# Optimization experiments

Measured on AMD Instinct MI355X. Metric: run time of the kernel, lower is better.

Reference implementation:

```python
import jax, jax.numpy as jnp
import numpy as np

NUM_EMB = 8192
DIM = 64
DECAY = 0.99
EPS = 1e-05
COMMIT = 0.25


def setup_inputs() -> dict:
    key = jax.random.key(0)
    k1, k2, k3 = jax.random.split(key, 3)
    inputs = jax.random.normal(k1, (8, 4096, DIM), jnp.float32)
    weight = jax.random.normal(k2, (NUM_EMB, DIM), jnp.float32)
    ema_cluster_count = jnp.ones((NUM_EMB,), jnp.float32)
    ema_weight_sum = jax.random.normal(k3, (NUM_EMB, DIM), jnp.float32)
    return {
        'inputs': inputs,
        'weight': weight,
        'ema_cluster_count': ema_cluster_count,
        'ema_weight_sum': ema_weight_sum,
    }


def reference(inputs, weight, ema_cluster_count, ema_weight_sum):
    flat = inputs.reshape(-1, DIM)  # [N, D]
    distances = (
        jnp.sum(flat ** 2, axis=1, keepdims=True)
        + jnp.sum(weight ** 2, axis=1)
        - 2.0 * flat @ weight.T
    )
    idx = jnp.argmin(distances, axis=1)  # [N] int

    # EMA stats (training branch): one-hot column sums == segment counts,
    # encodings.T @ flat == segment sums of inputs by code index.
    counts = jax.ops.segment_sum(
        jnp.ones(flat.shape[0], jnp.float32), idx, num_segments=NUM_EMB)
    new_cc = ema_cluster_count * DECAY + (1.0 - DECAY) * counts
    emb_sum = jax.ops.segment_sum(flat, idx, num_segments=NUM_EMB)
    new_ws = ema_weight_sum * DECAY + (1.0 - DECAY) * emb_sum

    n = jnp.sum(new_cc)
    smoothed = (new_cc + EPS) / (n + NUM_EMB * EPS) * n
    new_weight = new_ws / smoothed[:, None]  # updated codebook [K, D]

    quantized_raw = new_weight[idx].reshape(inputs.shape)
    e_latent_loss = jnp.mean((jax.lax.stop_gradient(quantized_raw) - inputs) ** 2)
    vq_loss = COMMIT * e_latent_loss

    avg_probs = counts / flat.shape[0]
    perplexity = jnp.exp(-jnp.sum(avg_probs * jnp.log(avg_probs + 1e-10)))

    # straight-through estimator
    quantized = inputs + jax.lax.stop_gradient(quantized_raw - inputs)
    return quantized, vq_loss, idx, perplexity, new_weight, new_cc, new_ws
```

## Files before the change

### kernel.cpp

```cpp
#include <hip/hip_runtime.h>
#include <math.h>

typedef _Float16 f16x8 __attribute__((ext_vector_type(8)));
typedef float f32x4 __attribute__((ext_vector_type(4)));

#define NROWS 32768
#define KEMB  8192

#define DECAYF 0.99f
#define OMDF   0.01f

#define OUT_Q    0
#define OUT_LOSS 2097152
#define OUT_IDX  2097153
#define OUT_PERP 2129921
#define OUT_NW   2129922
#define OUT_NCC  2654210
#define OUT_NWS  2662402

#define WS_N      0
#define WS_ENT    1
#define WS_COUNTS 4
#define WS_EMB    8196
#define WS_IDX    532484
#define WS_W2H    565252
#define WS_WFRAG  573444
#define WS_ZERO_UNITS 532484

__device__ __forceinline__ float sq_rn(float v) { return __fmul_rn(v, v); }

__device__ __forceinline__ float npsumsq64(const float* vbuf) {
  float a[8];
#pragma unroll
  for (int j = 0; j < 8; ++j) a[j] = sq_rn(vbuf[j]);
#pragma unroll
  for (int m = 1; m < 8; ++m)
#pragma unroll
    for (int j = 0; j < 8; ++j) a[j] = __fadd_rn(a[j], sq_rn(vbuf[m*8 + j]));
  return __fadd_rn(__fadd_rn(__fadd_rn(a[0],a[1]), __fadd_rn(a[2],a[3])),
                   __fadd_rn(__fadd_rn(a[4],a[5]), __fadd_rn(a[6],a[7])));
}

__device__ __forceinline__ void split_f16(float x, _Float16& hi, _Float16& lo) {
  hi = (_Float16)x;
  float r = __fsub_rn(x, (float)hi);
  lo = (_Float16)r;
}

__global__ __launch_bounds__(256) void prep_kernel(const float* __restrict__ wg,
                                                   float* __restrict__ ws) {
  const int tid = blockIdx.x * 256 + threadIdx.x;
  if (tid < KEMB) {
    const float* src = wg + (size_t)tid * 64;
    float vbuf[64];
#pragma unroll
    for (int f = 0; f < 16; ++f) {
      float4 v = *(const float4*)(src + f*4);
      vbuf[f*4+0]=v.x; vbuf[f*4+1]=v.y; vbuf[f*4+2]=v.z; vbuf[f*4+3]=v.w;
    }
    ws[WS_W2H + tid] = __fmul_rn(0.5f, npsumsq64(vbuf));
  } else if (tid < KEMB + 65536) {
    const int u = tid - KEMB;
    const int K = u >> 3, g = u & 7;
    const int n = K & 15, P = K >> 4;
    const int slot = (g&3)*16 + n, shi = g >> 2;
    const float* src = wg + (size_t)K*64 + g*8;
    float4 v0 = *(const float4*)src, v1 = *(const float4*)(src + 4);
    float vv[8] = {v0.x,v0.y,v0.z,v0.w,v1.x,v1.y,v1.z,v1.w};
    f16x8 hi, lo;
#pragma unroll
    for (int j = 0; j < 8; ++j) { _Float16 h, l; split_f16(vv[j], h, l); hi[j]=h; lo[j]=l; }
    _Float16* wf = (_Float16*)(ws + WS_WFRAG);
    *(f16x8*)&wf[((size_t)(P*4 + shi)*64 + slot)*8]     = hi;
    *(f16x8*)&wf[((size_t)(P*4 + 2 + shi)*64 + slot)*8] = lo;
  }
}

__global__ __launch_bounds__(512) void argmin_kernel(const float* __restrict__ xg,
                                                     float* __restrict__ out,
                                                     float* __restrict__ ws) {
  __shared__ __align__(16) _Float16 xp[8*4*64*8];
  __shared__ float md[128*4];
  __shared__ int   mk[128*4];

  const int t    = threadIdx.x;
  const int lane = t & 63, wv = t >> 6;
  const int quad = lane >> 4, n16 = lane & 15;
  const int rg = wv >> 2, cg = wv & 3;
  const int row0 = blockIdx.x * 128;
  const _Float16* __restrict__ wfrag = (const _Float16*)(ws + WS_WFRAG);
  const float* __restrict__ w2hg = ws + WS_W2H;

#pragma unroll
  for (int it = 0; it < 2; ++it) {
    const int u  = t + 512*it;
    const int rp = u >> 7, n = (u >> 3) & 15, g = u & 7;
    const float* src = xg + (size_t)(row0 + rp*16 + n)*64 + g*8;
    float4 v0 = *(const float4*)src, v1 = *(const float4*)(src + 4);
    float vv[8] = {v0.x,v0.y,v0.z,v0.w,v1.x,v1.y,v1.z,v1.w};
    f16x8 hi, lo;
#pragma unroll
    for (int j = 0; j < 8; ++j) { _Float16 h, l; split_f16(-vv[j], h, l); hi[j]=h; lo[j]=l; }
    const int slot = (g&3)*16 + n, shi = g >> 2;
    *(f16x8*)&xp[(((rp*4) + shi)*64 + slot)*8]     = hi;
    *(f16x8*)&xp[(((rp*4) + 2 + shi)*64 + slot)*8] = lo;
  }
  __syncthreads();

  f16x8 a[4][4];
#pragma unroll
  for (int rt = 0; rt < 4; ++rt)
#pragma unroll
    for (int s = 0; s < 4; ++s)
      a[rt][s] = *(const f16x8*)&xp[(((rg*4+rt)*4 + s)*64 + lane)*8];

  float best[16]; int bestk[16];
#pragma unroll
  for (int i = 0; i < 16; ++i) { best[i] = INFINITY; bestk[i] = 0; }

  const size_t lane8 = (size_t)lane * 8;
  f16x8 b0, b1, b2, b3;
  float w2;
  {
    const size_t base = ((size_t)(cg*4) * 64) * 8 + lane8;
    b0 = *(const f16x8*)&wfrag[base];
    b1 = *(const f16x8*)&wfrag[base + 512];
    b2 = *(const f16x8*)&wfrag[base + 1024];
    b3 = *(const f16x8*)&wfrag[base + 1536];
    w2 = w2hg[cg*16 + n16];
  }

  for (int it = 0; it < 128; ++it) {
    f16x8 n0, n1, n2, n3;
    float w2n;
    if (it < 127) {
      const size_t base = ((size_t)((it+1)*4 + cg) * 4 * 64) * 8 + lane8;
      n0 = *(const f16x8*)&wfrag[base];
      n1 = *(const f16x8*)&wfrag[base + 512];
      n2 = *(const f16x8*)&wfrag[base + 1024];
      n3 = *(const f16x8*)&wfrag[base + 1536];
      w2n = w2hg[(it+1)*64 + cg*16 + n16];
    }

    const f32x4 cin = {w2, w2, w2, w2};
    f32x4 acc[4];
#pragma unroll
    for (int rt = 0; rt < 4; ++rt) acc[rt] = __builtin_amdgcn_mfma_f32_16x16x32_f16(a[rt][0], b0, cin, 0,0,0);
#pragma unroll
    for (int rt = 0; rt < 4; ++rt) acc[rt] = __builtin_amdgcn_mfma_f32_16x16x32_f16(a[rt][1], b1, acc[rt], 0,0,0);
#pragma unroll
    for (int rt = 0; rt < 4; ++rt) acc[rt] = __builtin_amdgcn_mfma_f32_16x16x32_f16(a[rt][2], b0, acc[rt], 0,0,0);
#pragma unroll
    for (int rt = 0; rt < 4; ++rt) acc[rt] = __builtin_amdgcn_mfma_f32_16x16x32_f16(a[rt][3], b1, acc[rt], 0,0,0);
#pragma unroll
    for (int rt = 0; rt < 4; ++rt) acc[rt] = __builtin_amdgcn_mfma_f32_16x16x32_f16(a[rt][0], b2, acc[rt], 0,0,0);
#pragma unroll
    for (int rt = 0; rt < 4; ++rt) acc[rt] = __builtin_amdgcn_mfma_f32_16x16x32_f16(a[rt][1], b3, acc[rt], 0,0,0);
#pragma unroll
    for (int rt = 0; rt < 4; ++rt) acc[rt] = __builtin_amdgcn_mfma_f32_16x16x32_f16(a[rt][2], b2, acc[rt], 0,0,0);
#pragma unroll
    for (int rt = 0; rt < 4; ++rt) acc[rt] = __builtin_amdgcn_mfma_f32_16x16x32_f16(a[rt][3], b3, acc[rt], 0,0,0);

    const int kk = it*64 + cg*16 + n16;
#pragma unroll
    for (int rt = 0; rt < 4; ++rt)
#pragma unroll
      for (int reg = 0; reg < 4; ++reg) {
        const float dist = acc[rt][reg];
        const int bi = rt*4 + reg;
        if (dist < best[bi]) { best[bi] = dist; bestk[bi] = kk; }
      }

    b0 = n0; b1 = n1; b2 = n2; b3 = n3; w2 = w2n;
  }

#pragma unroll
  for (int bi = 0; bi < 16; ++bi) {
    float bd = best[bi]; int bk = bestk[bi];
#pragma unroll
    for (int m = 1; m < 16; m <<= 1) {
      const float od = __shfl_xor(bd, m, 64);
      const int   ok = __shfl_xor(bk, m, 64);
      if (od < bd || (od == bd && ok < bk)) { bd = od; bk = ok; }
    }
    best[bi] = bd; bestk[bi] = bk;
  }
  if (n16 == 0) {
#pragma unroll
    for (int rt = 0; rt < 4; ++rt)
#pragma unroll
      for (int reg = 0; reg < 4; ++reg) {
        const int row = rg*64 + rt*16 + quad*4 + reg;
        md[row*4 + cg] = best[rt*4+reg];
        mk[row*4 + cg] = bestk[rt*4+reg];
      }
  }
  __syncthreads();

  if (t < 128) {
    const int row = t;
    float bd = md[row*4]; int bk = mk[row*4];
#pragma unroll
    for (int u = 1; u < 4; ++u) {
      const float d2 = md[row*4 + u]; const int k2 = mk[row*4 + u];
      if (d2 < bd || (d2 == bd && k2 < bk)) { bd = d2; bk = k2; }
    }
    out[OUT_IDX + row0 + row] = (float)bk;
    ((int*)ws)[WS_IDX + row0 + row] = bk;
    atomicAdd(&ws[WS_COUNTS + bk], 1.0f);
  }
}

__global__ __launch_bounds__(256) void ema_kernel(const float* __restrict__ xg,
                                                  float* __restrict__ ws) {
  const int lane = threadIdx.x & 63, wv = threadIdx.x >> 6;
  const int base = blockIdx.x * 128 + wv * 32;
  const int* idxb = (const int*)ws + WS_IDX;
#pragma unroll 4
  for (int r = 0; r < 32; ++r) {
    const int row = base + r;
    const int k = idxb[row];
    atomicAdd(&ws[WS_EMB + (size_t)k*64 + lane], xg[(size_t)row*64 + lane]);
  }
}

__global__ __launch_bounds__(256) void stats_kernel(const float* __restrict__ cc,
                                                    float* __restrict__ out,
                                                    float* __restrict__ ws) {
  const int t = threadIdx.x;
  float v1 = 0.0f, v2 = 0.0f;
#pragma unroll
  for (int i = 0; i < 32; ++i) {
    const int k = i*256 + t;
    const float cnt = ws[WS_COUNTS + k];
    const float ncc = __fadd_rn(__fmul_rn(DECAYF, cc[k]), __fmul_rn(OMDF, cnt));
    out[OUT_NCC + k] = ncc;
    const float p = cnt * (1.0f/32768.0f);
    v1 += ncc;
    v2 += __fmul_rn(p, logf(__fadd_rn(p, 1e-10f)));
  }
#pragma unroll
  for (int off = 32; off > 0; off >>= 1) {
    v1 += __shfl_down(v1, off);
    v2 += __shfl_down(v2, off);
  }
  __shared__ float s1[4], s2[4];
  const int lane = t & 63, wid = t >> 6;
  if (lane == 0) { s1[wid] = v1; s2[wid] = v2; }
  __syncthreads();
  if (t == 0) {
    ws[WS_N]   = (s1[0]+s1[1]) + (s1[2]+s1[3]);
    ws[WS_ENT] = (s2[0]+s2[1]) + (s2[2]+s2[3]);
  }
}

__global__ __launch_bounds__(256) void update_kernel(const float* __restrict__ ws0,
                                                     float* __restrict__ out,
                                                     float* __restrict__ ws) {
  const int e = blockIdx.x * 256 + threadIdx.x;
  const int k = e >> 6;
  const float nws = __fadd_rn(__fmul_rn(DECAYF, ws0[e]), __fmul_rn(OMDF, ws[WS_EMB + e]));
  out[OUT_NWS + e] = nws;
  const float n = ws[WS_N];
  const float ncc = out[OUT_NCC + k];
  const float smoothed = __fmul_rn(__fadd_rn(ncc, 1e-5f) / __fadd_rn(n, 0.08192f), n);
  out[OUT_NW + e] = nws / smoothed;
  if (e == 0) out[OUT_PERP] = expf(-ws[WS_ENT]);
}

__global__ __launch_bounds__(256) void quant_kernel(const float* __restrict__ xg,
                                                    float* __restrict__ out,
                                                    float* __restrict__ ws) {
  const int t = threadIdx.x;
  const int* idxb = (const int*)ws + WS_IDX;
  float v = 0.0f;
#pragma unroll
  for (int j = 0; j < 4; ++j) {
    const int e4 = (j*512 + blockIdx.x)*256 + t;
    const int row = e4 >> 4, d = (e4 & 15) * 4;
    const int k = idxb[row];
    const float* nw = out + OUT_NW + (size_t)k*64 + d;
    float2 q0 = *(const float2*)nw, q1 = *(const float2*)(nw + 2);
    float4 x = *(const float4*)(xg + (size_t)e4*4);
    float qv[4] = {q0.x, q0.y, q1.x, q1.y};
    float xv[4] = {x.x, x.y, x.z, x.w};
    float4 o;
    float ov[4];
#pragma unroll
    for (int i = 0; i < 4; ++i) {
      const float df = __fsub_rn(qv[i], xv[i]);
      ov[i] = __fadd_rn(xv[i], df);
      v = fmaf(df, df, v);
    }
    o.x = ov[0]; o.y = ov[1]; o.z = ov[2]; o.w = ov[3];
    *(float4*)(out + OUT_Q + (size_t)e4*4) = o;
  }
#pragma unroll
  for (int off = 32; off > 0; off >>= 1) v += __shfl_down(v, off);
  __shared__ float sm[4];
  const int lane = t & 63, wid = t >> 6;
  if (lane == 0) sm[wid] = v;
  __syncthreads();
  if (t == 0) ws[WS_COUNTS + blockIdx.x] = (sm[0]+sm[1]) + (sm[2]+sm[3]);
}

__global__ void final_kernel(float* __restrict__ out, const float* __restrict__ ws) {
  const int t = threadIdx.x;
  float v = 0.0f;
#pragma unroll
  for (int i = 0; i < 8; ++i) v += ws[WS_COUNTS + i*64 + t];
#pragma unroll
  for (int off = 32; off > 0; off >>= 1) v += __shfl_down(v, off);
  if (t == 0) out[OUT_LOSS] = __fmul_rn(0.25f, v / 2097152.0f);
}

extern "C" void kernel_launch(void* const* d_in, const int* in_sizes, int n_in,
                              void* d_out, int out_size, void* d_ws, size_t ws_size,
                              hipStream_t stream) {
  (void)in_sizes; (void)n_in; (void)out_size; (void)ws_size;
  const float* x   = (const float*)d_in[0];
  const float* w   = (const float*)d_in[1];
  const float* cc  = (const float*)d_in[2];
  const float* ws0 = (const float*)d_in[3];
  float* out = (float*)d_out;
  float* ws  = (float*)d_ws;

  hipMemsetAsync(d_ws, 0, (size_t)WS_ZERO_UNITS * 4, stream);
  hipLaunchKernelGGL(prep_kernel,   dim3(288),  dim3(256), 0, stream, w, ws);
  hipLaunchKernelGGL(argmin_kernel, dim3(256),  dim3(512), 0, stream, x, out, ws);
  hipLaunchKernelGGL(ema_kernel,    dim3(256),  dim3(256), 0, stream, x, ws);
  hipLaunchKernelGGL(stats_kernel,  dim3(1),    dim3(256), 0, stream, cc, out, ws);
  hipLaunchKernelGGL(update_kernel, dim3(2048), dim3(256), 0, stream, ws0, out, ws);
  hipLaunchKernelGGL(quant_kernel,  dim3(512),  dim3(256), 0, stream, x, out, ws);
  hipLaunchKernelGGL(final_kernel,  dim3(1),    dim3(64),  0, stream, out, ws);
}
```

Baseline: 211.1 us.

## Drop lo*lo MFMA terms, unroll argmin loop, fuse EMA scatter, vectorize update

The argmin inner loop is unrolled by two with ping-pong register buffers for the codebook fragments. Each panel now issues six MFMA steps instead of eight, dropping the low-times-low products of the fp16 hi/lo split. This cuts matrix work by a quarter, at a small cost in distance accuracy that could flip near-tie argmins. The separate EMA segment-sum kernel is folded into the tail of the argmin kernel, using indices staged in shared memory. The update kernel now uses float4 loads and stores over a quarter of the blocks.

```diff
diff --git a/kernel.cpp b/kernel.cpp
--- a/kernel.cpp
+++ b/kernel.cpp
@@ -76,12 +76,50 @@
   }
 }
 
+#define COMPUTE_PANEL(I, B0, B1, B2, B3, W2)                                        \
+  {                                                                                 \
+    const f32x4 cin = {(W2), (W2), (W2), (W2)};                                     \
+    f32x4 acc[4];                                                                   \
+    _Pragma("unroll")                                                               \
+    for (int rt = 0; rt < 4; ++rt) acc[rt] = __builtin_amdgcn_mfma_f32_16x16x32_f16(a[rt][0], (B0), cin, 0,0,0); \
+    _Pragma("unroll")                                                               \
+    for (int rt = 0; rt < 4; ++rt) acc[rt] = __builtin_amdgcn_mfma_f32_16x16x32_f16(a[rt][1], (B1), acc[rt], 0,0,0); \
+    _Pragma("unroll")                                                               \
+    for (int rt = 0; rt < 4; ++rt) acc[rt] = __builtin_amdgcn_mfma_f32_16x16x32_f16(a[rt][2], (B0), acc[rt], 0,0,0); \
+    _Pragma("unroll")                                                               \
+    for (int rt = 0; rt < 4; ++rt) acc[rt] = __builtin_amdgcn_mfma_f32_16x16x32_f16(a[rt][3], (B1), acc[rt], 0,0,0); \
+    _Pragma("unroll")                                                               \
+    for (int rt = 0; rt < 4; ++rt) acc[rt] = __builtin_amdgcn_mfma_f32_16x16x32_f16(a[rt][0], (B2), acc[rt], 0,0,0); \
+    _Pragma("unroll")                                                               \
+    for (int rt = 0; rt < 4; ++rt) acc[rt] = __builtin_amdgcn_mfma_f32_16x16x32_f16(a[rt][1], (B3), acc[rt], 0,0,0); \
+    const int kk = (I)*64 + cg*16 + n16;                                            \
+    _Pragma("unroll")                                                               \
+    for (int rt = 0; rt < 4; ++rt)                                                  \
+      _Pragma("unroll")                                                             \
+      for (int reg = 0; reg < 4; ++reg) {                                           \
+        const float dist = acc[rt][reg];                                            \
+        const int bi = rt*4 + reg;                                                  \
+        if (dist < best[bi]) { best[bi] = dist; bestk[bi] = kk; }                   \
+      }                                                                             \
+  }
+
+#define LOADB(I, C0, C1, C2, C3, CW)                                                \
+  {                                                                                 \
+    const size_t base = ((size_t)((I)*4 + cg) * 256) * 8 + lane8;                   \
+    C0 = *(const f16x8*)&wfrag[base];                                               \
+    C1 = *(const f16x8*)&wfrag[base + 512];                                         \
+    C2 = *(const f16x8*)&wfrag[base + 1024];                                        \
+    C3 = *(const f16x8*)&wfrag[base + 1536];                                        \
+    CW = w2hg[(I)*64 + cg*16 + n16];                                                \
+  }
+
 __global__ __launch_bounds__(512) void argmin_kernel(const float* __restrict__ xg,
                                                      float* __restrict__ out,
                                                      float* __restrict__ ws) {
   __shared__ __align__(16) _Float16 xp[8*4*64*8];
   __shared__ float md[128*4];
   __shared__ int   mk[128*4];
+  __shared__ int   bkL[128];
 
   const int t    = threadIdx.x;
   const int lane = t & 63, wv = t >> 6;
@@ -119,59 +157,15 @@
   for (int i = 0; i < 16; ++i) { best[i] = INFINITY; bestk[i] = 0; }
 
   const size_t lane8 = (size_t)lane * 8;
-  f16x8 b0, b1, b2, b3;
-  float w2;
-  {
-    const size_t base = ((size_t)(cg*4) * 64) * 8 + lane8;
-    b0 = *(const f16x8*)&wfrag[base];
-    b1 = *(const f16x8*)&wfrag[base + 512];
-    b2 = *(const f16x8*)&wfrag[base + 1024];
-    b3 = *(const f16x8*)&wfrag[base + 1536];
-    w2 = w2hg[cg*16 + n16];
-  }
-
-  for (int it = 0; it < 128; ++it) {
-    f16x8 n0, n1, n2, n3;
-    float w2n;
-    if (it < 127) {
-      const size_t base = ((size_t)((it+1)*4 + cg) * 4 * 64) * 8 + lane8;
-      n0 = *(const f16x8*)&wfrag[base];
-      n1 = *(const f16x8*)&wfrag[base + 512];
-      n2 = *(const f16x8*)&wfrag[base + 1024];
-      n3 = *(const f16x8*)&wfrag[base + 1536];
-      w2n = w2hg[(it+1)*64 + cg*16 + n16];
-    }
-
-    const f32x4 cin = {w2, w2, w2, w2};
-    f32x4 acc[4];
-#pragma unroll
-    for (int rt = 0; rt < 4; ++rt) acc[rt] = __builtin_amdgcn_mfma_f32_16x16x32_f16(a[rt][0], b0, cin, 0,0,0);
-#pragma unroll
-    for (int rt = 0; rt < 4; ++rt) acc[rt] = __builtin_amdgcn_mfma_f32_16x16x32_f16(a[rt][1], b1, acc[rt], 0,0,0);
-#pragma unroll
-    for (int rt = 0; rt < 4; ++rt) acc[rt] = __builtin_amdgcn_mfma_f32_16x16x32_f16(a[rt][2], b0, acc[rt], 0,0,0);
-#pragma unroll
-    for (int rt = 0; rt < 4; ++rt) acc[rt] = __builtin_amdgcn_mfma_f32_16x16x32_f16(a[rt][3], b1, acc[rt], 0,0,0);
-#pragma unroll
-    for (int rt = 0; rt < 4; ++rt) acc[rt] = __builtin_amdgcn_mfma_f32_16x16x32_f16(a[rt][0], b2, acc[rt], 0,0,0);
-#pragma unroll
-    for (int rt = 0; rt < 4; ++rt) acc[rt] = __builtin_amdgcn_mfma_f32_16x16x32_f16(a[rt][1], b3, acc[rt], 0,0,0);
-#pragma unroll
-    for (int rt = 0; rt < 4; ++rt) acc[rt] = __builtin_amdgcn_mfma_f32_16x16x32_f16(a[rt][2], b2, acc[rt], 0,0,0);
-#pragma unroll
-    for (int rt = 0; rt < 4; ++rt) acc[rt] = __builtin_amdgcn_mfma_f32_16x16x32_f16(a[rt][3], b3, acc[rt], 0,0,0);
-
-    const int kk = it*64 + cg*16 + n16;
-#pragma unroll
-    for (int rt = 0; rt < 4; ++rt)
-#pragma unroll
-      for (int reg = 0; reg < 4; ++reg) {
-        const float dist = acc[rt][reg];
-        const int bi = rt*4 + reg;
-        if (dist < best[bi]) { best[bi] = dist; bestk[bi] = kk; }
-      }
-
-    b0 = n0; b1 = n1; b2 = n2; b3 = n3; w2 = w2n;
+  f16x8 p0, p1, p2, p3, q0, q1, q2, q3;
+  float pw, qw;
+  LOADB(0, p0, p1, p2, p3, pw);
+
+  for (int it = 0; it < 128; it += 2) {
+    LOADB(it+1, q0, q1, q2, q3, qw);
+    COMPUTE_PANEL(it, p0, p1, p2, p3, pw);
+    if (it + 2 < 128) LOADB(it+2, p0, p1, p2, p3, pw);
+    COMPUTE_PANEL(it+1, q0, q1, q2, q3, qw);
   }
 
 #pragma unroll
@@ -207,20 +201,17 @@
     }
     out[OUT_IDX + row0 + row] = (float)bk;
     ((int*)ws)[WS_IDX + row0 + row] = bk;
+    bkL[row] = bk;
     atomicAdd(&ws[WS_COUNTS + bk], 1.0f);
   }
-}
-
-__global__ __launch_bounds__(256) void ema_kernel(const float* __restrict__ xg,
-                                                  float* __restrict__ ws) {
-  const int lane = threadIdx.x & 63, wv = threadIdx.x >> 6;
-  const int base = blockIdx.x * 128 + wv * 32;
-  const int* idxb = (const int*)ws + WS_IDX;
+  __syncthreads();
+
 #pragma unroll 4
-  for (int r = 0; r < 32; ++r) {
-    const int row = base + r;
-    const int k = idxb[row];
-    atomicAdd(&ws[WS_EMB + (size_t)k*64 + lane], xg[(size_t)row*64 + lane]);
+  for (int r = 0; r < 16; ++r) {
+    const int row = wv*16 + r;
+    const int k = bkL[row];
+    atomicAdd(&ws[WS_EMB + (size_t)k*64 + lane],
+              xg[(size_t)(row0 + row)*64 + lane]);
   }
 }
 
@@ -257,15 +248,28 @@
 __global__ __launch_bounds__(256) void update_kernel(const float* __restrict__ ws0,
                                                      float* __restrict__ out,
                                                      float* __restrict__ ws) {
-  const int e = blockIdx.x * 256 + threadIdx.x;
-  const int k = e >> 6;
-  const float nws = __fadd_rn(__fmul_rn(DECAYF, ws0[e]), __fmul_rn(OMDF, ws[WS_EMB + e]));
-  out[OUT_NWS + e] = nws;
+  const int e4 = blockIdx.x * 256 + threadIdx.x;
+  const int k = e4 >> 4;
   const float n = ws[WS_N];
   const float ncc = out[OUT_NCC + k];
   const float smoothed = __fmul_rn(__fadd_rn(ncc, 1e-5f) / __fadd_rn(n, 0.08192f), n);
-  out[OUT_NW + e] = nws / smoothed;
-  if (e == 0) out[OUT_PERP] = expf(-ws[WS_ENT]);
+  const float inv_s = 1.0f / smoothed;
+  float4 w0 = *(const float4*)(ws0 + (size_t)e4*4);
+  float4 em = *(const float4*)(ws + WS_EMB + (size_t)e4*4);
+  float wv[4] = {w0.x, w0.y, w0.z, w0.w};
+  float ev[4] = {em.x, em.y, em.z, em.w};
+  float nwsv[4], nwv[4];
+#pragma unroll
+  for (int i = 0; i < 4; ++i) {
+    nwsv[i] = __fadd_rn(__fmul_rn(DECAYF, wv[i]), __fmul_rn(OMDF, ev[i]));
+    nwv[i]  = nwsv[i] / smoothed;
+  }
+  (void)inv_s;
+  float4 onws = {nwsv[0], nwsv[1], nwsv[2], nwsv[3]};
+  float4 onw  = {nwv[0],  nwv[1],  nwv[2],  nwv[3]};
+  *(float4*)(out + OUT_NWS + (size_t)e4*4) = onws;
+  *(float4*)(out + OUT_NW  + (size_t)e4*4) = onw;
+  if (e4 == 0) out[OUT_PERP] = expf(-ws[WS_ENT]);
 }
 
 __global__ __launch_bounds__(256) void quant_kernel(const float* __restrict__ xg,
@@ -328,9 +332,8 @@
   hipMemsetAsync(d_ws, 0, (size_t)WS_ZERO_UNITS * 4, stream);
   hipLaunchKernelGGL(prep_kernel,   dim3(288),  dim3(256), 0, stream, w, ws);
   hipLaunchKernelGGL(argmin_kernel, dim3(256),  dim3(512), 0, stream, x, out, ws);
-  hipLaunchKernelGGL(ema_kernel,    dim3(256),  dim3(256), 0, stream, x, ws);
   hipLaunchKernelGGL(stats_kernel,  dim3(1),    dim3(256), 0, stream, cc, out, ws);
-  hipLaunchKernelGGL(update_kernel, dim3(2048), dim3(256), 0, stream, ws0, out, ws);
+  hipLaunchKernelGGL(update_kernel, dim3(512),  dim3(256), 0, stream, ws0, out, ws);
   hipLaunchKernelGGL(quant_kernel,  dim3(512),  dim3(256), 0, stream, x, out, ws);
   hipLaunchKernelGGL(final_kernel,  dim3(1),    dim3(64),  0, stream, out, ws);
 }
```

Result: faster. 187.8 us (-11.1%).
